# Performance work log

Measured on AMD Instinct MI355X. Metric: run time of the kernel, lower is better.

Reference implementation:

```python
import jax, jax.numpy as jnp
import numpy as np

R_EPS = 1e-15

def _sdf_net(x, W1, b1, W2, b2):
    h = jax.nn.relu(x @ W1 + b1)
    return h @ W2 + b2  # [..., 1+feat]

def _fd_gradient(x, W1, b1, W2, b2, eps):
    # central finite differences of the SDF along the 3 axes
    offs = eps * jnp.eye(3, dtype=x.dtype)              # [3,3]
    xp = x[None, :, :] + offs[:, None, :]               # [3,P,3]
    xm = x[None, :, :] - offs[:, None, :]
    sp = _sdf_net(xp, W1, b1, W2, b2)[..., 0]           # [3,P]
    sm = _sdf_net(xm, W1, b1, W2, b2)[..., 0]
    return ((sp - sm) / (2.0 * eps)).T                  # [P,3]

def _softplus100(x):
    # torch.nn.Softplus(beta=100)
    return jax.nn.softplus(100.0 * x) / 100.0

def _exclusive_cumprod(a):
    ones = jnp.ones_like(a[:, :1])
    return jnp.cumprod(jnp.concatenate([ones, a], -1), -1)[:, :-1]

def _sample_pdf(bins, weights, n_samples):
    # bins [R,K], weights [R,K-1]; deterministic inverse-CDF sampling (det=True)
    weights = weights + 1e-5
    pdf = weights / jnp.sum(weights, -1, keepdims=True)
    cdf = jnp.cumsum(pdf, -1)
    cdf = jnp.concatenate([jnp.zeros_like(cdf[:, :1]), cdf], -1)  # [R,K]
    K = cdf.shape[-1]
    u = jnp.linspace(0.5 / n_samples, 1.0 - 0.5 / n_samples, n_samples, dtype=bins.dtype)
    u = jnp.broadcast_to(u[None], (bins.shape[0], n_samples))
    inds = jax.vmap(lambda c, uu: jnp.searchsorted(c, uu, side='right'))(cdf, u)
    below = jnp.clip(inds - 1, 0, K - 1)
    above = jnp.clip(inds, 0, K - 1)
    cdf_b = jnp.take_along_axis(cdf, below, -1)
    cdf_a = jnp.take_along_axis(cdf, above, -1)
    bin_b = jnp.take_along_axis(bins, below, -1)
    bin_a = jnp.take_along_axis(bins, above, -1)
    denom = cdf_a - cdf_b
    denom = jnp.where(denom < 1e-5, jnp.ones_like(denom), denom)
    t = (u - cdf_b) / denom
    return bin_b + t * (bin_a - bin_b)

def _forward(rays_o, rays_d, W1, b1, W2, b2, Wc1, bc1, Wc2, bc2, inv_s_param,
             num_steps, upsample_steps, bound):
    B, N = rays_o.shape[:2]
    ro = rays_o.reshape(-1, 3)
    rd = rays_d.reshape(-1, 3)
    R = ro.shape[0]
    bnd = float(bound)
    # near/far from cube bound
    tmin = (-bnd - ro) / (rd + R_EPS)
    tmax = (bnd - ro) / (rd + R_EPS)
    near = jnp.max(jnp.minimum(tmin, tmax), -1, keepdims=True)
    far = jnp.min(jnp.maximum(tmin, tmax), -1, keepdims=True)
    near = jnp.maximum(near, 0.05)
    z = jnp.linspace(0.0, 1.0, num_steps, dtype=ro.dtype)[None]
    z_vals = near + (far - near) * z                     # [R,S0]
    sample_dist = (far - near) / num_steps               # [R,1]
    pts = ro[:, None, :] + rd[:, None, :] * z_vals[..., None]
    pts = jnp.clip(pts, -bnd, bnd)
    # --- coarse SDF pass + inverse-CDF importance resampling (torch.no_grad) ---
    sdf_c = _sdf_net(pts.reshape(-1, 3), W1, b1, W2, b2)[:, 0].reshape(R, num_steps)
    sdf_c = jax.lax.stop_gradient(sdf_c)
    d_c = z_vals[:, 1:] - z_vals[:, :-1]
    mid_sdf = 0.5 * (sdf_c[:, 1:] + sdf_c[:, :-1])
    cos_val = jnp.clip((sdf_c[:, 1:] - sdf_c[:, :-1]) / (d_c + 1e-5), -1e3, 0.0)
    prev_c = jax.nn.sigmoid((mid_sdf - cos_val * d_c * 0.5) * 64.0)
    next_c = jax.nn.sigmoid((mid_sdf + cos_val * d_c * 0.5) * 64.0)
    alpha_c = jnp.clip((prev_c - next_c + 1e-5) / (prev_c + 1e-5), 0.0, 1.0)
    w_c = alpha_c * _exclusive_cumprod(1.0 - alpha_c + 1e-7)
    new_z = jax.lax.stop_gradient(_sample_pdf(z_vals, w_c, upsample_steps))
    z_vals = jnp.sort(jnp.concatenate([z_vals, new_z], -1), -1)
    S = num_steps + upsample_steps
    # --- fine pass: deltas / midpoints / shading / NeuS compositing ---
    deltas = z_vals[:, 1:] - z_vals[:, :-1]
    deltas = jnp.concatenate([deltas, jnp.broadcast_to(sample_dist, (R, 1))], -1)
    z_mid = jnp.concatenate([z_vals[:, :-1] + 0.5 * deltas[:, :-1], z_vals[:, -1:]], -1)
    new_pts = ro[:, None, :] + rd[:, None, :] * z_mid[..., None]
    new_pts = jnp.clip(new_pts, -bnd, bnd)
    flat_pts = new_pts.reshape(-1, 3)                    # [R*S,3]
    out = _sdf_net(flat_pts, W1, b1, W2, b2)
    sdf = out[:, :1]
    feat = out[:, 1:]
    grad = _fd_gradient(flat_pts, W1, b1, W2, b2, 0.005)  # eps=0.005*(1-ratio), ratio=0
    normal = grad / (1e-5 + jnp.linalg.norm(grad, axis=-1, keepdims=True))
    dirs = jnp.broadcast_to(rd[:, None, :], new_pts.shape).reshape(-1, 3)
    cin = jnp.concatenate([flat_pts, dirs, normal, feat], -1)
    color = jax.nn.sigmoid(jax.nn.relu(cin @ Wc1 + bc1) @ Wc2 + bc2)   # [R*S,3]
    inv_s = jnp.exp(10.0 * inv_s_param)                   # forward_variance()
    true_cos = jnp.sum(dirs * normal, -1, keepdims=True)
    iter_cos = -_softplus100(-true_cos)                   # cos_anneal_ratio = 1.0
    d_flat = deltas.reshape(-1, 1)
    prev_cdf = jax.nn.sigmoid((sdf - iter_cos * d_flat * 0.5) * inv_s)
    next_cdf = jax.nn.sigmoid((sdf + iter_cos * d_flat * 0.5) * inv_s)
    alpha = jnp.clip((prev_cdf - next_cdf + 1e-5) / (prev_cdf + 1e-5), 0.0, 1.0).reshape(R, S)
    weights = alpha * _exclusive_cumprod(1.0 - alpha + 1e-7)
    weights_sum = jnp.sum(weights, -1, keepdims=True)
    image = jnp.sum(color.reshape(R, S, 3) * weights[..., None], 1)
    image = image + (1.0 - weights_sum) * 1.0             # bg_color = 1
    return image.reshape(B, N, 3)

def setup_inputs() -> dict:
    key = jax.random.key(0)
    ks = jax.random.split(key, 8)
    B, N, H, F = 1, 4096, 64, 64
    rays_o = (jax.random.uniform(ks[0], (B, N, 3), jnp.float32) - 0.5) * 0.5
    d = jax.random.normal(ks[1], (B, N, 3), jnp.float32)
    rays_d = d / (1e-8 + jnp.linalg.norm(d, axis=-1, keepdims=True))
    def lin(k, i, o):
        return jax.random.normal(k, (i, o), jnp.float32) / np.sqrt(i).astype(np.float32)
    W1 = lin(ks[2], 3, H); b1 = jnp.zeros((H,), jnp.float32)
    W2 = lin(ks[3], H, 1 + F); b2 = jnp.zeros((1 + F,), jnp.float32)
    Wc1 = lin(ks[4], 9 + F, H); bc1 = jnp.zeros((H,), jnp.float32)
    Wc2 = lin(ks[5], H, 3); bc2 = jnp.zeros((3,), jnp.float32)
    inv_s_param = jnp.full((1,), 0.3, jnp.float32)
    return {"rays_o": rays_o, "rays_d": rays_d, "W1": W1, "b1": b1, "W2": W2, "b2": b2,
            "Wc1": Wc1, "bc1": bc1, "Wc2": Wc2, "bc2": bc2, "inv_s_param": inv_s_param,
            "num_steps": 64, "upsample_steps": 64, "bound": 1}

def reference(rays_o, rays_d, W1, b1, W2, b2, Wc1, bc1, Wc2, bc2, inv_s_param,
              num_steps, upsample_steps, bound):
    return _forward(rays_o, rays_d, W1, b1, W2, b2, Wc1, bc1, Wc2, bc2, inv_s_param,
                    num_steps, upsample_steps, bound)
```

## Files before the change

kernel.cpp:

```cpp
#include <hip/hip_runtime.h>
#include <hip/hip_bf16.h>
#include <cmath>

#define RAYS_PER_BLOCK 2
#define KS 84

#define OFF_W1    0
#define OFF_W1E   256
#define OFF_W1S   512
#define OFF_WC2   768
#define OFF_BC2   1024
#define OFF_GC    1028
#define OFF_AF    1032

typedef __attribute__((ext_vector_type(4))) short  short4v;
typedef __attribute__((ext_vector_type(8))) short  short8v;
typedef __attribute__((ext_vector_type(16))) float f32x16;

__device__ __forceinline__ float sigm(float x){ return 1.0f/(1.0f + expf(-x)); }
__device__ __forceinline__ float clampf(float x, float lo, float hi){ return fminf(fmaxf(x, lo), hi); }
__device__ __forceinline__ unsigned short f2bf(float x){
  __hip_bfloat16 h = __float2bfloat16(x);
  return *reinterpret_cast<unsigned short*>(&h);
}
__device__ __forceinline__ unsigned pk2(float a, float b){
  return (unsigned)f2bf(a) | ((unsigned)f2bf(b) << 16);
}
__device__ __forceinline__ short8v lds_load8(const unsigned short* p){
  short4v lo = *(const short4v*)p;
  short4v hi = *(const short4v*)(p + 4);
  short8v r;
  r[0]=lo[0]; r[1]=lo[1]; r[2]=lo[2]; r[3]=lo[3];
  r[4]=hi[0]; r[5]=hi[1]; r[6]=hi[2]; r[7]=hi[3];
  return r;
}

__global__ __launch_bounds__(256)
void prep_weights(const float* __restrict__ W1, const float* __restrict__ b1,
                  const float* __restrict__ W2, const float* __restrict__ b2,
                  const float* __restrict__ Wc1, const float* __restrict__ bc1,
                  const float* __restrict__ Wc2, const float* __restrict__ bc2,
                  float* __restrict__ ws)
{
  __shared__ unsigned short W2T[64*KS];
  __shared__ unsigned short ABUF[64*KS];
  const int tid  = threadIdx.x;
  const int lane = tid & 63;
  const int wv   = tid >> 6;
  const int l31  = lane & 31;
  const int h    = lane >> 5;

  for (int i = tid; i < 4096; i += 256){
    int k = i >> 6, t = i & 63;
    W2T[k*KS + t] = f2bf(W2[k*65 + 1 + t]);
  }
  for (int i = tid; i < 576; i += 256){
    int ii = i >> 6, c = i & 63;
    ABUF[c*KS + 64 + ii] = f2bf(Wc1[ii*64 + c]);
  }
  for (int i = tid; i < 384; i += 256){
    int z = i >> 6, c = i & 63;
    ABUF[c*KS + 74 + z] = 0;
  }
  if (wv == 3){
    float acc = bc1[lane];
    #pragma unroll 4
    for (int t = 0; t < 64; ++t) acc = fmaf(b2[1+t], Wc1[(9+t)*64 + lane], acc);
    ABUF[lane*KS + 73] = f2bf(acc);
  }
  if (tid < 64){
    int j = tid;
    float wx = W1[j], wy = W1[64+j], wz = W1[128+j];
    float w2 = W2[j*65];
    float Hx = 0.005f * fabsf(wx);
    float Hy = 0.005f * fabsf(wy);
    float Hz = 0.005f * fabsf(wz);
    float Sx = (wx < 0.f) ? -w2 : w2;
    float Sy = (wy < 0.f) ? -w2 : w2;
    float Sz = (wz < 0.f) ? -w2 : w2;
    ws[OFF_W1 + 4*j + 0] = wx;
    ws[OFF_W1 + 4*j + 1] = wy;
    ws[OFF_W1 + 4*j + 2] = wz;
    ws[OFF_W1 + 4*j + 3] = b1[j];
    ws[OFF_W1E + 4*j + 0] = Hx;
    ws[OFF_W1E + 4*j + 1] = Hy;
    ws[OFF_W1E + 4*j + 2] = Hz;
    ws[OFF_W1E + 4*j + 3] = w2;
    ws[OFF_W1S + 4*j + 0] = Sx;
    ws[OFF_W1S + 4*j + 1] = Sy;
    ws[OFF_W1S + 4*j + 2] = Sz;
    ws[OFF_W1S + 4*j + 3] = 0.f;
    float sx = Sx*Hx, sy = Sy*Hy, sz = Sz*Hz;
    #pragma unroll
    for (int off = 1; off < 64; off <<= 1){
      sx += __shfl_xor(sx, off);
      sy += __shfl_xor(sy, off);
      sz += __shfl_xor(sz, off);
    }
    if (j == 0){
      ws[OFF_GC + 0] = sx;
      ws[OFF_GC + 1] = sy;
      ws[OFF_GC + 2] = sz;
    }
  } else if (tid < 128){
    int j = tid - 64;
    ws[OFF_WC2 + 4*j + 0] = Wc2[j*3+0];
    ws[OFF_WC2 + 4*j + 1] = Wc2[j*3+1];
    ws[OFF_WC2 + 4*j + 2] = Wc2[j*3+2];
    ws[OFF_WC2 + 4*j + 3] = 0.f;
  } else if (tid < 132){
    int j = tid - 128;
    ws[OFF_BC2 + j] = (j < 3) ? bc2[j] : b2[0];
  }
  __syncthreads();

  {
    const int mb = wv & 1, kb = wv >> 1;
    f32x16 e;
    #pragma unroll
    for (int i = 0; i < 16; ++i) e[i] = 0.f;
    #pragma unroll
    for (int s = 0; s < 4; ++s){
      short8v afr;
      #pragma unroll
      for (int j = 0; j < 8; ++j)
        afr[j] = (short)f2bf(Wc1[(9 + 16*s + 8*h + j)*64 + 32*mb + l31]);
      short8v bfr = lds_load8(&W2T[(32*kb + l31)*KS + 16*s + 8*h]);
      e = __builtin_amdgcn_mfma_f32_32x32x16_bf16(afr, bfr, e, 0, 0, 0);
    }
    const int kcol = 32*kb + l31;
    #pragma unroll
    for (int r = 0; r < 16; ++r){
      int c = 32*mb + (r & 3) + 8*(r >> 2) + 4*h;
      ABUF[c*KS + kcol] = f2bf(e[r]);
    }
  }
  __syncthreads();

  for (int i = tid; i < 640; i += 256){
    int f = i >> 6, ln = i & 63;
    int mb = f / 5, kk = f - 5*mb;
    int c  = 32*mb + (ln & 31);
    int kb2 = 16*kk + 8*(ln >> 5);
    short8v v = lds_load8(&ABUF[c*KS + kb2]);
    *((short8v*)(((unsigned short*)(ws + OFF_AF)) + (size_t)i * 8)) = v;
  }
}

__global__ __launch_bounds__(256)
void neus_render(const float* __restrict__ rays_o, const float* __restrict__ rays_d,
                 const float* __restrict__ inv_s_p, const float* __restrict__ ws,
                 float* __restrict__ out)
{
  __shared__ unsigned short s_aext[4][64*KS];
  __shared__ float4 s_wc2[64];
  __shared__ __align__(16) float s_wobwd[RAYS_PER_BLOCK][128];
  __shared__ float  s_z[RAYS_PER_BLOCK][64];
  __shared__ float  s_cdf[RAYS_PER_BLOCK][64];
  __shared__ float  s_newz[RAYS_PER_BLOCK][64];
  __shared__ float  s_zall[RAYS_PER_BLOCK][128];
  __shared__ float  s_red[RAYS_PER_BLOCK][2][4];
  __shared__ float  s_wtot[RAYS_PER_BLOCK][2];

  const int tid  = threadIdx.x;
  const int rs   = tid >> 7;
  const int lt   = tid & 127;
  const int lane = tid & 63;
  const int wir  = (tid >> 6) & 1;
  const int wv   = tid >> 6;
  const int ray  = blockIdx.x * RAYS_PER_BLOCK + rs;

  const float4* __restrict__ pW1  = (const float4*)(ws + OFF_W1);
  const float4* __restrict__ pW1E = (const float4*)(ws + OFF_W1E);
  const float4* __restrict__ pW1S = (const float4*)(ws + OFF_W1S);
  const float*  __restrict__ pbc2 = ws + OFF_BC2;
  const float*  __restrict__ pgc  = ws + OFF_GC;
  const float b20 = pbc2[3];

  if (tid < 64) s_wc2[tid] = ((const float4*)(ws + OFF_WC2))[tid];

  float ox = rays_o[ray*3], oy = rays_o[ray*3+1], oz = rays_o[ray*3+2];
  float dx = rays_d[ray*3], dy = rays_d[ray*3+1], dz = rays_d[ray*3+2];
  float tnx = (-1.f-ox)/(dx+1e-15f), tfx = (1.f-ox)/(dx+1e-15f);
  float tny = (-1.f-oy)/(dy+1e-15f), tfy = (1.f-oy)/(dy+1e-15f);
  float tnz = (-1.f-oz)/(dz+1e-15f), tfz = (1.f-oz)/(dz+1e-15f);
  float nearv = fmaxf(fmaxf(fminf(tnx,tfx), fminf(tny,tfy)), fminf(tnz,tfz));
  float farv  = fminf(fminf(fmaxf(tnx,tfx), fmaxf(tny,tfy)), fmaxf(tnz,tfz));
  nearv = fmaxf(nearv, 0.05f);
  const float sd = (farv - nearv) * (1.f/64.f);

  if (wir == 1){
    float4 wj = pW1[lane];
    float wob = fmaf(ox, wj.x, fmaf(oy, wj.y, fmaf(oz, wj.z, wj.w)));
    float wd  = fmaf(dx, wj.x, fmaf(dy, wj.y, dz*wj.z));
    s_wobwd[rs][2*lane]   = wob;
    s_wobwd[rs][2*lane+1] = wd;
  }
  __syncthreads();

  if (wir == 0){
    float zt = nearv + (farv-nearv) * ((float)lane * (1.f/63.f));
    const float2* wb2 = (const float2*)s_wobwd[rs];
    float acc = b20;
    #pragma unroll 8
    for (int j = 0; j < 64; ++j){
      float2 q = wb2[j];
      acc = fmaf(fmaxf(fmaf(zt, q.y, q.x), 0.f), ws[OFF_W1E + 4*j + 3], acc);
    }
    s_z[rs][lane] = zt;
    float s1  = __shfl_down(acc, 1);
    float zt1 = nearv + (farv-nearv) * ((float)(lane+1) * (1.f/63.f));
    float a_c = 0.f, qv = 1.f;
    if (lane < 63){
      float dc   = zt1 - zt;
      float mid  = 0.5f*(acc + s1);
      float cosv = clampf((s1-acc)/(dc+1e-5f), -1000.f, 0.f);
      float est  = cosv*dc*0.5f;
      float pcv  = sigm((mid-est)*64.f);
      float ncv  = sigm((mid+est)*64.f);
      a_c = clampf((pcv-ncv+1e-5f)/(pcv+1e-5f), 0.f, 1.f);
      qv  = 1.f - a_c + 1e-7f;
    }
    float p = qv;
    #pragma unroll
    for (int off = 1; off < 64; off <<= 1){
      float t = __shfl_up(p, off);
      if (lane >= off) p *= t;
    }
    float ec = __shfl_up(p, 1);
    if (lane == 0) ec = 1.f;
    float wvv = (lane < 63) ? (a_c*ec + 1e-5f) : 0.f;
    float tot = wvv;
    #pragma unroll
    for (int off = 32; off > 0; off >>= 1) tot += __shfl_xor(tot, off);
    float cs = wvv;
    #pragma unroll
    for (int off = 1; off < 64; off <<= 1){
      float t = __shfl_up(cs, off);
      if (lane >= off) cs += t;
    }
    if (lane == 0)  s_cdf[rs][0] = 0.f;
    if (lane < 63)  s_cdf[rs][lane+1] = cs / tot;
  }
  __syncthreads();

  if (wir == 0){
    float u = ((float)lane + 0.5f) * (1.f/64.f);
    int lo = 0, hi = 64;
    while (lo < hi){
      int m = (lo+hi) >> 1;
      if (s_cdf[rs][m] <= u) lo = m+1; else hi = m;
    }
    int below = lo - 1;
    int above = lo < 63 ? lo : 63;
    float cb = s_cdf[rs][below], ca = s_cdf[rs][above];
    float bb = s_z[rs][below],   ba = s_z[rs][above];
    float den = ca - cb; if (den < 1e-5f) den = 1.f;
    float tt = (u - cb)/den;
    s_newz[rs][lane] = bb + tt*(ba - bb);
  }
  __syncthreads();

  const short8v* pAF = (const short8v*)(ws + OFF_AF);
  short8v af[10];
  #pragma unroll
  for (int f = 0; f < 10; ++f) af[f] = pAF[f*64 + lane];

  {
    float v; int pos;
    if (lt < 64){
      v = s_z[rs][lt];
      int lo = 0, hi = 64;
      while (lo < hi){ int m=(lo+hi)>>1; if (s_newz[rs][m] < v) lo = m+1; else hi = m; }
      pos = lt + lo;
    } else {
      int jj = lt - 64;
      v = s_newz[rs][jj];
      int lo = 0, hi = 64;
      while (lo < hi){ int m=(lo+hi)>>1; if (s_z[rs][m] <= v) lo = m+1; else hi = m; }
      pos = jj + lo;
    }
    s_zall[rs][pos] = v;
  }
  __syncthreads();

  float zc = s_zall[rs][lt];
  float zn = s_zall[rs][lt < 127 ? lt+1 : 127];
  float delta = (lt < 127) ? (zn - zc) : sd;
  float zm    = (lt < 127) ? (zc + 0.5f*delta) : zc;
  float px = clampf(ox + dx*zm, -1.f, 1.f);
  float py = clampf(oy + dy*zm, -1.f, 1.f);
  float pz = clampf(oz + dz*zm, -1.f, 1.f);

  unsigned short* arow = &s_aext[wv][(unsigned)lane * KS];
  const float4* wb4 = (const float4*)s_wobwd[rs];
  float sa = b20;
  float gxa = pgc[0], gya = pgc[1], gza = pgc[2];
  #pragma unroll 4
  for (int p = 0; p < 32; ++p){
    float4 q  = wb4[p];
    float4 e0 = pW1E[2*p],   s0 = pW1S[2*p];
    float4 e1 = pW1E[2*p+1], s1v = pW1S[2*p+1];
    float base0 = fmaf(zm, q.y, q.x);
    float base1 = fmaf(zm, q.w, q.z);
    float hv0 = fmaxf(base0, 0.f), hv1 = fmaxf(base1, 0.f);
    sa = fmaf(hv0, e0.w, sa); sa = fmaf(hv1, e1.w, sa);
    gxa = fmaf(__builtin_amdgcn_fmed3f(base0, -e0.x, e0.x), s0.x, gxa);
    gya = fmaf(__builtin_amdgcn_fmed3f(base0, -e0.y, e0.y), s0.y, gya);
    gza = fmaf(__builtin_amdgcn_fmed3f(base0, -e0.z, e0.z), s0.z, gza);
    gxa = fmaf(__builtin_amdgcn_fmed3f(base1, -e1.x, e1.x), s1v.x, gxa);
    gya = fmaf(__builtin_amdgcn_fmed3f(base1, -e1.y, e1.y), s1v.y, gya);
    gza = fmaf(__builtin_amdgcn_fmed3f(base1, -e1.z, e1.z), s1v.z, gza);
    *(unsigned*)&arow[2*p] = pk2(hv0, hv1);
  }
  float sdfv = sa;
  float gx = gxa*100.f, gy = gya*100.f, gz = gza*100.f;
  float gn = 1e-5f + sqrtf(gx*gx + gy*gy + gz*gz);
  float nx = gx/gn, ny = gy/gn, nz = gz/gn;

  *(unsigned*)&arow[64] = pk2(px, py);
  *(unsigned*)&arow[66] = pk2(pz, dx);
  *(unsigned*)&arow[68] = pk2(dy, dz);
  *(unsigned*)&arow[70] = pk2(nx, ny);
  *(unsigned*)&arow[72] = pk2(nz, 1.0f);
  *(unsigned*)&arow[74] = 0u;
  *(unsigned*)&arow[76] = 0u;
  *(unsigned*)&arow[78] = 0u;

  const float inv_s = expf(10.f * inv_s_p[0]);
  float tcos = dx*nx + dy*ny + dz*nz;
  float aarg = -100.f * tcos;
  float spv  = (aarg > 0.f) ? (aarg + log1pf(expf(-aarg))) : log1pf(expf(aarg));
  float iter_cos = -(spv * 0.01f);
  float est = iter_cos * delta * 0.5f;
  float pcv = sigm((sdfv - est)*inv_s);
  float ncv = sigm((sdfv + est)*inv_s);
  float alpha = clampf((pcv - ncv + 1e-5f)/(pcv + 1e-5f), 0.f, 1.f);

  float qv = 1.f - alpha + 1e-7f;
  float p = qv;
  #pragma unroll
  for (int off = 1; off < 64; off <<= 1){
    float t = __shfl_up(p, off);
    if (lane >= off) p *= t;
  }
  if (lane == 63) s_wtot[rs][wir] = p;
  __syncthreads();
  float excl = __shfl_up(p, 1);
  if (lane == 0) excl = 1.f;
  if (wir == 1) excl *= s_wtot[rs][0];
  float w  = alpha * excl;

  f32x16 acc00, acc01, acc10, acc11;
  #pragma unroll
  for (int i = 0; i < 16; ++i){ acc00[i]=0.f; acc01[i]=0.f; acc10[i]=0.f; acc11[i]=0.f; }
  const unsigned short* aw = s_aext[wv];
  const int scol = lane & 31;
  const int half8 = (lane >> 5) * 8;
  #pragma unroll
  for (int kk = 0; kk < 5; ++kk){
    int koff = 16*kk + half8;
    short8v b0 = lds_load8(&aw[ scol      * KS + koff]);
    short8v b1 = lds_load8(&aw[(32+scol) * KS + koff]);
    acc00 = __builtin_amdgcn_mfma_f32_32x32x16_bf16(af[kk],   b0, acc00, 0, 0, 0);
    acc10 = __builtin_amdgcn_mfma_f32_32x32x16_bf16(af[5+kk], b0, acc10, 0, 0, 0);
    acc01 = __builtin_amdgcn_mfma_f32_32x32x16_bf16(af[kk],   b1, acc01, 0, 0, 0);
    acc11 = __builtin_amdgcn_mfma_f32_32x32x16_bf16(af[5+kk], b1, acc11, 0, 0, 0);
  }

  float pr0=0.f,pr1=0.f,pr2=0.f,pr3=0.f,pr4=0.f,pr5=0.f;
  const int halfoff = (lane >> 5) * 4;
  #pragma unroll
  for (int r = 0; r < 16; ++r){
    int ci = (r & 3) + 8*(r >> 2) + halfoff;
    float4 wA = s_wc2[ci];
    float4 wB = s_wc2[32 + ci];
    float v;
    v = fmaxf(acc00[r], 0.f); pr0 = fmaf(v, wA.x, pr0); pr1 = fmaf(v, wA.y, pr1); pr2 = fmaf(v, wA.z, pr2);
    v = fmaxf(acc10[r], 0.f); pr0 = fmaf(v, wB.x, pr0); pr1 = fmaf(v, wB.y, pr1); pr2 = fmaf(v, wB.z, pr2);
    v = fmaxf(acc01[r], 0.f); pr3 = fmaf(v, wA.x, pr3); pr4 = fmaf(v, wA.y, pr4); pr5 = fmaf(v, wA.z, pr5);
    v = fmaxf(acc11[r], 0.f); pr3 = fmaf(v, wB.x, pr3); pr4 = fmaf(v, wB.y, pr4); pr5 = fmaf(v, wB.z, pr5);
  }
  pr0 += __shfl_xor(pr0, 32); pr1 += __shfl_xor(pr1, 32); pr2 += __shfl_xor(pr2, 32);
  pr3 += __shfl_xor(pr3, 32); pr4 += __shfl_xor(pr4, 32); pr5 += __shfl_xor(pr5, 32);
  const bool hihalf = (lane >= 32);
  float c0 = sigm((hihalf ? pr3 : pr0) + pbc2[0]);
  float c1 = sigm((hihalf ? pr4 : pr1) + pbc2[1]);
  float c2 = sigm((hihalf ? pr5 : pr2) + pbc2[2]);

  float r0 = w, r1 = w*c0, r2 = w*c1, r3 = w*c2;
  #pragma unroll
  for (int off = 32; off > 0; off >>= 1){
    r0 += __shfl_xor(r0, off);
    r1 += __shfl_xor(r1, off);
    r2 += __shfl_xor(r2, off);
    r3 += __shfl_xor(r3, off);
  }
  if (lane == 0){
    s_red[rs][wir][0]=r0; s_red[rs][wir][1]=r1; s_red[rs][wir][2]=r2; s_red[rs][wir][3]=r3;
  }
  __syncthreads();
  if (lt == 0){
    float wsum = s_red[rs][0][0] + s_red[rs][1][0];
    float bg = 1.f - wsum;
    out[ray*3+0] = s_red[rs][0][1] + s_red[rs][1][1] + bg;
    out[ray*3+1] = s_red[rs][0][2] + s_red[rs][1][2] + bg;
    out[ray*3+2] = s_red[rs][0][3] + s_red[rs][1][3] + bg;
  }
}

extern "C" void kernel_launch(void* const* d_in, const int* in_sizes, int n_in,
                              void* d_out, int out_size, void* d_ws, size_t ws_size,
                              hipStream_t stream)
{
  const float* rays_o = (const float*)d_in[0];
  const float* rays_d = (const float*)d_in[1];
  const float* W1  = (const float*)d_in[2];
  const float* b1  = (const float*)d_in[3];
  const float* W2  = (const float*)d_in[4];
  const float* b2  = (const float*)d_in[5];
  const float* Wc1 = (const float*)d_in[6];
  const float* bc1 = (const float*)d_in[7];
  const float* Wc2 = (const float*)d_in[8];
  const float* bc2 = (const float*)d_in[9];
  const float* inv_s = (const float*)d_in[10];
  float* out = (float*)d_out;
  float* ws  = (float*)d_ws;

  prep_weights<<<1, 256, 0, stream>>>(W1, b1, W2, b2, Wc1, bc1, Wc2, bc2, ws);

  const int R = in_sizes[0] / 3;
  dim3 grid(R / RAYS_PER_BLOCK), block(256);
  neus_render<<<grid, block, 0, stream>>>(rays_o, rays_d, inv_s, ws, out);
}
```

Measured before the change: 134.8 us.

## Process one ray per 128-thread block and drop per-ray wob/wd precompute

Changes the decomposition from two rays per 256-thread block to one ray per 128-thread block, halving shared memory per block and adding a min-blocks launch bound to raise occupancy. It also removes the per-ray precompute of W1·o and W1·d into shared memory (and its barrier). Instead each sample point is clamped to the cube and W1 is applied directly to it. That adds VALU work per hidden unit and changes semantics: the old path computed on unclamped points while the new one clamps. Smaller blocks mean more blocks to schedule, with less synchronisation contention per block.

```diff
diff --git a/kernel.cpp b/kernel.cpp
--- a/kernel.cpp
+++ b/kernel.cpp
@@ -2,7 +2,6 @@
 #include <hip/hip_bf16.h>
 #include <cmath>
 
-#define RAYS_PER_BLOCK 2
 #define KS 84
 
 #define OFF_W1    0
@@ -147,28 +146,25 @@
   }
 }
 
-__global__ __launch_bounds__(256)
+__global__ __launch_bounds__(128, 3)
 void neus_render(const float* __restrict__ rays_o, const float* __restrict__ rays_d,
                  const float* __restrict__ inv_s_p, const float* __restrict__ ws,
                  float* __restrict__ out)
 {
-  __shared__ unsigned short s_aext[4][64*KS];
+  __shared__ unsigned short s_aext[2][64*KS];
   __shared__ float4 s_wc2[64];
-  __shared__ __align__(16) float s_wobwd[RAYS_PER_BLOCK][128];
-  __shared__ float  s_z[RAYS_PER_BLOCK][64];
-  __shared__ float  s_cdf[RAYS_PER_BLOCK][64];
-  __shared__ float  s_newz[RAYS_PER_BLOCK][64];
-  __shared__ float  s_zall[RAYS_PER_BLOCK][128];
-  __shared__ float  s_red[RAYS_PER_BLOCK][2][4];
-  __shared__ float  s_wtot[RAYS_PER_BLOCK][2];
+  __shared__ float  s_z[64];
+  __shared__ float  s_cdf[64];
+  __shared__ float  s_newz[64];
+  __shared__ float  s_zall[128];
+  __shared__ float  s_red[2][4];
+  __shared__ float  s_wtot[2];
 
   const int tid  = threadIdx.x;
-  const int rs   = tid >> 7;
-  const int lt   = tid & 127;
+  const int lt   = tid;
   const int lane = tid & 63;
-  const int wir  = (tid >> 6) & 1;
-  const int wv   = tid >> 6;
-  const int ray  = blockIdx.x * RAYS_PER_BLOCK + rs;
+  const int wir  = tid >> 6;
+  const int ray  = blockIdx.x;
 
   const float4* __restrict__ pW1  = (const float4*)(ws + OFF_W1);
   const float4* __restrict__ pW1E = (const float4*)(ws + OFF_W1E);
@@ -189,25 +185,18 @@
   nearv = fmaxf(nearv, 0.05f);
   const float sd = (farv - nearv) * (1.f/64.f);
 
-  if (wir == 1){
-    float4 wj = pW1[lane];
-    float wob = fmaf(ox, wj.x, fmaf(oy, wj.y, fmaf(oz, wj.z, wj.w)));
-    float wd  = fmaf(dx, wj.x, fmaf(dy, wj.y, dz*wj.z));
-    s_wobwd[rs][2*lane]   = wob;
-    s_wobwd[rs][2*lane+1] = wd;
-  }
-  __syncthreads();
-
   if (wir == 0){
     float zt = nearv + (farv-nearv) * ((float)lane * (1.f/63.f));
-    const float2* wb2 = (const float2*)s_wobwd[rs];
+    float px = clampf(ox + dx*zt, -1.f, 1.f);
+    float py = clampf(oy + dy*zt, -1.f, 1.f);
+    float pz = clampf(oz + dz*zt, -1.f, 1.f);
     float acc = b20;
     #pragma unroll 8
     for (int j = 0; j < 64; ++j){
-      float2 q = wb2[j];
-      acc = fmaf(fmaxf(fmaf(zt, q.y, q.x), 0.f), ws[OFF_W1E + 4*j + 3], acc);
-    }
-    s_z[rs][lane] = zt;
+      float4 w = pW1[j];
+      acc += fmaxf(px*w.x + py*w.y + pz*w.z + w.w, 0.f) * ws[OFF_W1E + 4*j + 3];
+    }
+    s_z[lane] = zt;
     float s1  = __shfl_down(acc, 1);
     float zt1 = nearv + (farv-nearv) * ((float)(lane+1) * (1.f/63.f));
     float a_c = 0.f, qv = 1.f;
@@ -239,8 +228,8 @@
       float t = __shfl_up(cs, off);
       if (lane >= off) cs += t;
     }
-    if (lane == 0)  s_cdf[rs][0] = 0.f;
-    if (lane < 63)  s_cdf[rs][lane+1] = cs / tot;
+    if (lane == 0)  s_cdf[0] = 0.f;
+    if (lane < 63)  s_cdf[lane+1] = cs / tot;
   }
   __syncthreads();
 
@@ -249,15 +238,15 @@
     int lo = 0, hi = 64;
     while (lo < hi){
       int m = (lo+hi) >> 1;
-      if (s_cdf[rs][m] <= u) lo = m+1; else hi = m;
+      if (s_cdf[m] <= u) lo = m+1; else hi = m;
     }
     int below = lo - 1;
     int above = lo < 63 ? lo : 63;
-    float cb = s_cdf[rs][below], ca = s_cdf[rs][above];
-    float bb = s_z[rs][below],   ba = s_z[rs][above];
+    float cb = s_cdf[below], ca = s_cdf[above];
+    float bb = s_z[below],   ba = s_z[above];
     float den = ca - cb; if (den < 1e-5f) den = 1.f;
     float tt = (u - cb)/den;
-    s_newz[rs][lane] = bb + tt*(ba - bb);
+    s_newz[lane] = bb + tt*(ba - bb);
   }
   __syncthreads();
 
@@ -269,40 +258,39 @@
   {
     float v; int pos;
     if (lt < 64){
-      v = s_z[rs][lt];
+      v = s_z[lt];
       int lo = 0, hi = 64;
-      while (lo < hi){ int m=(lo+hi)>>1; if (s_newz[rs][m] < v) lo = m+1; else hi = m; }
+      while (lo < hi){ int m=(lo+hi)>>1; if (s_newz[m] < v) lo = m+1; else hi = m; }
       pos = lt + lo;
     } else {
       int jj = lt - 64;
-      v = s_newz[rs][jj];
+      v = s_newz[jj];
       int lo = 0, hi = 64;
-      while (lo < hi){ int m=(lo+hi)>>1; if (s_z[rs][m] <= v) lo = m+1; else hi = m; }
+      while (lo < hi){ int m=(lo+hi)>>1; if (s_z[m] <= v) lo = m+1; else hi = m; }
       pos = jj + lo;
     }
-    s_zall[rs][pos] = v;
-  }
-  __syncthreads();
-
-  float zc = s_zall[rs][lt];
-  float zn = s_zall[rs][lt < 127 ? lt+1 : 127];
+    s_zall[pos] = v;
+  }
+  __syncthreads();
+
+  float zc = s_zall[lt];
+  float zn = s_zall[lt < 127 ? lt+1 : 127];
   float delta = (lt < 127) ? (zn - zc) : sd;
   float zm    = (lt < 127) ? (zc + 0.5f*delta) : zc;
   float px = clampf(ox + dx*zm, -1.f, 1.f);
   float py = clampf(oy + dy*zm, -1.f, 1.f);
   float pz = clampf(oz + dz*zm, -1.f, 1.f);
 
-  unsigned short* arow = &s_aext[wv][(unsigned)lane * KS];
-  const float4* wb4 = (const float4*)s_wobwd[rs];
+  unsigned short* arow = &s_aext[wir][(unsigned)lane * KS];
   float sa = b20;
   float gxa = pgc[0], gya = pgc[1], gza = pgc[2];
-  #pragma unroll 4
-  for (int p = 0; p < 32; ++p){
-    float4 q  = wb4[p];
-    float4 e0 = pW1E[2*p],   s0 = pW1S[2*p];
-    float4 e1 = pW1E[2*p+1], s1v = pW1S[2*p+1];
-    float base0 = fmaf(zm, q.y, q.x);
-    float base1 = fmaf(zm, q.w, q.z);
+  #pragma unroll 2
+  for (int j2 = 0; j2 < 32; ++j2){
+    int j = 2*j2;
+    float4 w0 = pW1[j],   e0 = pW1E[j],   s0 = pW1S[j];
+    float4 w1 = pW1[j+1], e1 = pW1E[j+1], s1v = pW1S[j+1];
+    float base0 = fmaf(px, w0.x, fmaf(py, w0.y, fmaf(pz, w0.z, w0.w)));
+    float base1 = fmaf(px, w1.x, fmaf(py, w1.y, fmaf(pz, w1.z, w1.w)));
     float hv0 = fmaxf(base0, 0.f), hv1 = fmaxf(base1, 0.f);
     sa = fmaf(hv0, e0.w, sa); sa = fmaf(hv1, e1.w, sa);
     gxa = fmaf(__builtin_amdgcn_fmed3f(base0, -e0.x, e0.x), s0.x, gxa);
@@ -311,7 +299,7 @@
     gxa = fmaf(__builtin_amdgcn_fmed3f(base1, -e1.x, e1.x), s1v.x, gxa);
     gya = fmaf(__builtin_amdgcn_fmed3f(base1, -e1.y, e1.y), s1v.y, gya);
     gza = fmaf(__builtin_amdgcn_fmed3f(base1, -e1.z, e1.z), s1v.z, gza);
-    *(unsigned*)&arow[2*p] = pk2(hv0, hv1);
+    *(unsigned*)&arow[j] = pk2(hv0, hv1);
   }
   float sdfv = sa;
   float gx = gxa*100.f, gy = gya*100.f, gz = gza*100.f;
@@ -344,17 +332,17 @@
     float t = __shfl_up(p, off);
     if (lane >= off) p *= t;
   }
-  if (lane == 63) s_wtot[rs][wir] = p;
+  if (lane == 63) s_wtot[wir] = p;
   __syncthreads();
   float excl = __shfl_up(p, 1);
   if (lane == 0) excl = 1.f;
-  if (wir == 1) excl *= s_wtot[rs][0];
+  if (wir == 1) excl *= s_wtot[0];
   float w  = alpha * excl;
 
   f32x16 acc00, acc01, acc10, acc11;
   #pragma unroll
   for (int i = 0; i < 16; ++i){ acc00[i]=0.f; acc01[i]=0.f; acc10[i]=0.f; acc11[i]=0.f; }
-  const unsigned short* aw = s_aext[wv];
+  const unsigned short* aw = s_aext[wir];
   const int scol = lane & 31;
   const int half8 = (lane >> 5) * 8;
   #pragma unroll
@@ -397,15 +385,15 @@
     r3 += __shfl_xor(r3, off);
   }
   if (lane == 0){
-    s_red[rs][wir][0]=r0; s_red[rs][wir][1]=r1; s_red[rs][wir][2]=r2; s_red[rs][wir][3]=r3;
-  }
-  __syncthreads();
-  if (lt == 0){
-    float wsum = s_red[rs][0][0] + s_red[rs][1][0];
+    s_red[wir][0]=r0; s_red[wir][1]=r1; s_red[wir][2]=r2; s_red[wir][3]=r3;
+  }
+  __syncthreads();
+  if (tid == 0){
+    float wsum = s_red[0][0] + s_red[1][0];
     float bg = 1.f - wsum;
-    out[ray*3+0] = s_red[rs][0][1] + s_red[rs][1][1] + bg;
-    out[ray*3+1] = s_red[rs][0][2] + s_red[rs][1][2] + bg;
-    out[ray*3+2] = s_red[rs][0][3] + s_red[rs][1][3] + bg;
+    out[ray*3+0] = s_red[0][1] + s_red[1][1] + bg;
+    out[ray*3+1] = s_red[0][2] + s_red[1][2] + bg;
+    out[ray*3+2] = s_red[0][3] + s_red[1][3] + bg;
   }
 }
 
@@ -430,6 +418,6 @@
   prep_weights<<<1, 256, 0, stream>>>(W1, b1, W2, b2, Wc1, bc1, Wc2, bc2, ws);
 
   const int R = in_sizes[0] / 3;
-  dim3 grid(R / RAYS_PER_BLOCK), block(256);
+  dim3 grid(R), block(128);
   neus_render<<<grid, block, 0, stream>>>(rays_o, rays_d, inv_s, ws, out);
 }
```

Result: no change. 132.3 us (-1.8%).
